# Performance work log

Hardware: AMD Instinct MI355X
Metric: run time of the kernel (lower is better)

## Reference

```python
import jax, jax.numpy as jnp
import numpy as np

B, N, M, K, S, P, H, W = 8, 32, 32, 3, 1, 1, 192, 192
NH = (H + 2 * P - K) // S + 1
NW = (W + 2 * P - K) // S + 1


def setup_inputs() -> dict:
    key = jax.random.key(0)
    ks = jax.random.split(key, 8)
    f = lambda k, sh, sc: jax.random.normal(k, sh, jnp.float32) * sc
    return {
        "x": f(ks[0], (B, N, H, W), 1.0),
        "a1_w": f(ks[1], (K * K, N, K, K), 0.05),  # attention1 conv k x k
        "a1_b": jnp.zeros((K * K,), jnp.float32),
        "a2_w": f(ks[2], (K * K, K * K), 0.1),      # attention1 1x1 conv
        "a2_b": jnp.zeros((K * K,), jnp.float32),
        "a3_w": f(ks[3], (K * K, K * K), 0.1),      # attention1 1x1 conv
        "a3_b": jnp.zeros((K * K,), jnp.float32),
        "b1_w": f(ks[4], (M, N), 0.05),             # attention3 1x1 conv
        "b1_b": jnp.zeros((M,), jnp.float32),
        "b2_w": f(ks[5], (M, M), 0.05),             # attention3 1x1 conv
        "b2_b": jnp.zeros((M,), jnp.float32),
        "weight": f(ks[6], (M, N, K, K), 0.05),     # main conv weight
    }


def _attention1(x, a1_w, a1_b, a2_w, a2_b, a3_w, a3_b):
    # Conv(k) -> ReLU -> Conv1x1 -> ReLU -> Conv1x1 -> Sigmoid; out [B, K*K, NH, NW]
    a = jax.lax.conv_general_dilated(
        x, a1_w, (S, S), [(P, P), (P, P)],
        dimension_numbers=("NCHW", "OIHW", "NCHW"))
    a = jax.nn.relu(a + a1_b[None, :, None, None])
    a = jax.nn.relu(jnp.einsum("oi,bihw->bohw", a2_w, a) + a2_b[None, :, None, None])
    a = jnp.einsum("oi,bihw->bohw", a3_w, a) + a3_b[None, :, None, None]
    return jax.nn.sigmoid(a)


def _unfold(x):
    # torch F.unfold ordering: channel-major, kernel positions inner.
    # returns [B, N, K*K, NH, NW]
    xp = jnp.pad(x, ((0, 0), (0, 0), (P, P), (P, P)))
    cols = [xp[:, :, i:i + (NH - 1) * S + 1:S, j:j + (NW - 1) * S + 1:S]
            for i in range(K) for j in range(K)]
    return jnp.stack(cols, axis=2)


def reference(x, a1_w, a1_b, a2_w, a2_b, a3_w, a3_b, b1_w, b1_b, b2_w, b2_b, weight):
    att = _attention1(x, a1_w, a1_b, a2_w, a2_b, a3_w, a3_b)  # [B, K*K, NH, NW]
    pat = _unfold(x)                                          # [B, N, K*K, NH, NW]
    w = weight.reshape(M, N, K * K)
    # attention-weighted unfold + matmul + fold, fused as one einsum
    y = jnp.einsum("bnphw,bphw,mnp->bmhw", pat, att, w)       # [B, M, NH, NW]
    # attention3 bias: global avg pool -> 1x1 -> ReLU -> 1x1
    pooled = x.mean(axis=(2, 3))                              # [B, N]
    h = jax.nn.relu(pooled @ b1_w.T + b1_b)
    bias = h @ b2_w.T + b2_b                                  # [B, M]
    return y + bias[:, :, None, None]
```

## Files before the change

### kernel.cpp

```cpp
#include <hip/hip_runtime.h>
#include <math.h>

#define B_ 8
#define N_ 32
#define M_ 32
#define HW 192

typedef __attribute__((ext_vector_type(8))) short short8;
typedef __attribute__((ext_vector_type(4))) float float4_;

__device__ inline unsigned short f2bf(float f) {
    unsigned int b = __float_as_uint(f);
    b += 0x7FFF + ((b >> 16) & 1);
    return (unsigned short)(b >> 16);
}
__device__ inline float bf2f(unsigned short u) {
    return __uint_as_float((unsigned int)u << 16);
}

union U8 { short8 s; unsigned int u[4]; };

__global__ __launch_bounds__(256) void pool_prep_kernel(
    const float* __restrict__ x, const float* __restrict__ a1w,
    const float* __restrict__ weight, float* __restrict__ pooled,
    unsigned short* __restrict__ a1A, unsigned short* __restrict__ wA) {
    if (blockIdx.x == 256) {
        int tid = threadIdx.x;
        for (int idx = tid; idx < 9 * 512; idx += 256) {
            int j = idx & 7, l = (idx >> 3) & 63, c = idx >> 9;
            int o = l & 15, n = (l >> 4) * 8 + j;
            float v = (o < 9) ? a1w[(o * N_ + n) * 9 + c] : 0.f;
            a1A[idx] = f2bf(v);
        }
        for (int idx = tid; idx < 9 * 1024; idx += 256) {
            int j = idx & 7, l = (idx >> 3) & 63, mt = (idx >> 9) & 1, c = idx >> 10;
            int m = mt * 16 + (l & 15), n = (l >> 4) * 8 + j;
            wA[idx] = f2bf(weight[(m * N_ + n) * 9 + c]);
        }
        return;
    }
    int bn = blockIdx.x;
    const float4_* p = (const float4_*)(x + (size_t)bn * (HW * HW));
    float s = 0.f;
    for (int i = threadIdx.x; i < (HW * HW) / 4; i += 256) {
        float4_ v = p[i];
        s += (v[0] + v[1]) + (v[2] + v[3]);
    }
#pragma unroll
    for (int off = 32; off > 0; off >>= 1) s += __shfl_down(s, off, 64);
    __shared__ float red[4];
    if ((threadIdx.x & 63) == 0) red[threadIdx.x >> 6] = s;
    __syncthreads();
    if (threadIdx.x == 0)
        pooled[bn] = (red[0] + red[1] + red[2] + red[3]) * (1.f / (HW * HW));
}

__global__ __launch_bounds__(256) void laconv_kernel(
    const float* __restrict__ x, const float* __restrict__ a1b,
    const float* __restrict__ a2w, const float* __restrict__ a2b,
    const float* __restrict__ a3w, const float* __restrict__ a3b,
    const unsigned short* __restrict__ a1A, const unsigned short* __restrict__ wA,
    const float* __restrict__ pooled, const float* __restrict__ b1w,
    const float* __restrict__ b1b, const float* __restrict__ b2w,
    const float* __restrict__ b2b, float* __restrict__ out) {
    __shared__ __align__(16) unsigned short xs[324 * 40];
    __shared__ unsigned short att_s[9 * 264];
    __shared__ float hsh[M_];
    __shared__ __align__(16) float bias_lds[M_];

    const int id = blockIdx.x;
    const int b = id & 7;
    const int t = id >> 3;
    const int bx = t % 12, by = t / 12;
    const int th0 = by * 16, tw0 = bx * 16;
    const int tid = threadIdx.x;
    const int wv = tid >> 6, lane = tid & 63;
    const int tx = lane & 15, ks = lane >> 4;
    const float* xb = x + (size_t)b * N_ * HW * HW;

    float fv[5][8];
    int posv[5], grpv[5];
#pragma unroll
    for (int it0 = 0; it0 < 5; ++it0) {
        int it = tid + it0 * 256;
        int grp = it / 324;
        int pos = it - grp * 324;
        posv[it0] = pos; grpv[it0] = grp;
        int r = pos / 18, cc = pos - r * 18;
        int h = th0 + r - 1, wc = tw0 + cc - 1;
        const float* src = xb + (size_t)(grp * 8) * (HW * HW) + h * HW + wc;
        if (((unsigned)h < HW) && ((unsigned)wc < HW)) {
#pragma unroll
            for (int i = 0; i < 8; ++i) fv[it0][i] = src[i * (HW * HW)];
        } else {
#pragma unroll
            for (int i = 0; i < 8; ++i) fv[it0][i] = 0.f;
        }
    }
    float fr[8];
    int posr = 0;
    if (tid < 16) {
        int it = 1280 + tid;
        int pos = it - 3 * 324;
        posr = pos;
        int r = pos / 18, cc = pos - r * 18;
        int h = th0 + r - 1, wc = tw0 + cc - 1;
        const float* src = xb + (size_t)24 * (HW * HW) + h * HW + wc;
        if (((unsigned)h < HW) && ((unsigned)wc < HW)) {
#pragma unroll
            for (int i = 0; i < 8; ++i) fr[i] = src[i * (HW * HW)];
        } else {
#pragma unroll
            for (int i = 0; i < 8; ++i) fr[i] = 0.f;
        }
    }
#pragma unroll
    for (int it0 = 0; it0 < 5; ++it0) {
        U8 tt;
#pragma unroll
        for (int i = 0; i < 4; ++i)
            tt.u[i] = (unsigned)f2bf(fv[it0][2 * i]) |
                      ((unsigned)f2bf(fv[it0][2 * i + 1]) << 16);
        *(short8*)&xs[posv[it0] * 40 + grpv[it0] * 8] = tt.s;
    }
    if (tid < 16) {
        U8 tt;
#pragma unroll
        for (int i = 0; i < 4; ++i)
            tt.u[i] = (unsigned)f2bf(fr[2 * i]) | ((unsigned)f2bf(fr[2 * i + 1]) << 16);
        *(short8*)&xs[posr * 40 + 24] = tt.s;
    }
    if (tid < M_) {
        float s = b1b[tid];
#pragma unroll
        for (int n = 0; n < N_; n++) s += pooled[b * N_ + n] * b1w[tid * N_ + n];
        hsh[tid] = fmaxf(s, 0.f);
    }
    __syncthreads();
    if (tid < M_) {
        float s2 = b2b[tid];
#pragma unroll
        for (int q = 0; q < M_; q++) s2 += hsh[q] * b2w[tid * M_ + q];
        bias_lds[tid] = s2;
    }

    const int pb = (wv * 4) * 720 + tx * 40 + ks * 8;
    const float4_ zero4 = {0.f, 0.f, 0.f, 0.f};

    float4_ aacc[4];
#pragma unroll
    for (int g = 0; g < 4; ++g) aacc[g] = zero4;
#pragma unroll
    for (int c = 0; c < 9; ++c) {
        short8 aA = ((const short8*)a1A)[c * 64 + lane];
        const int coff = (c / 3) * 720 + (c % 3) * 40;
#pragma unroll
        for (int g = 0; g < 4; ++g) {
            short8 bP = *(const short8*)&xs[pb + g * 720 + coff];
            aacc[g] = __builtin_amdgcn_mfma_f32_16x16x32_bf16(aA, bP, aacc[g], 0, 0, 0);
        }
    }
#pragma unroll
    for (int g = 0; g < 4; ++g) {
#pragma unroll
        for (int reg = 0; reg < 4; ++reg) {
            int o = ks * 4 + reg;
            if (o < 9) att_s[o * 264 + (wv * 4 + g) * 16 + tx] = f2bf(aacc[g][reg]);
        }
    }
    __syncthreads();

    float t1[9], t2[9], attv[9];
#pragma unroll
    for (int o = 0; o < 9; ++o)
        t1[o] = fmaxf(bf2f(att_s[o * 264 + tid]) + a1b[o], 0.f);
#pragma unroll
    for (int o2 = 0; o2 < 9; ++o2) {
        float s = a2b[o2];
#pragma unroll
        for (int o = 0; o < 9; ++o) s += a2w[o2 * 9 + o] * t1[o];
        t2[o2] = fmaxf(s, 0.f);
    }
#pragma unroll
    for (int o3 = 0; o3 < 9; ++o3) {
        float s = a3b[o3];
#pragma unroll
        for (int o2 = 0; o2 < 9; ++o2) s += a3w[o3 * 9 + o2] * t2[o2];
        attv[o3] = 1.f / (1.f + __expf(-s));
    }
#pragma unroll
    for (int p = 0; p < 9; ++p) att_s[p * 264 + tid] = f2bf(attv[p]);
    __syncthreads();

    float4_ acc0[4], acc1[4];
#pragma unroll
    for (int g = 0; g < 4; ++g) { acc0[g] = zero4; acc1[g] = zero4; }
#pragma unroll
    for (int c = 0; c < 9; ++c) {
        short8 w0 = ((const short8*)wA)[c * 128 + lane];
        short8 w1 = ((const short8*)wA)[c * 128 + 64 + lane];
        const int coff = (c / 3) * 720 + (c % 3) * 40;
#pragma unroll
        for (int g = 0; g < 4; ++g) {
            short8 bP = *(const short8*)&xs[pb + g * 720 + coff];
            float av = bf2f(att_s[c * 264 + (wv * 4 + g) * 16 + tx]);
            float4_ av4 = {av, av, av, av};
            float4_ z0 = __builtin_amdgcn_mfma_f32_16x16x32_bf16(w0, bP, zero4, 0, 0, 0);
            float4_ z1 = __builtin_amdgcn_mfma_f32_16x16x32_bf16(w1, bP, zero4, 0, 0, 0);
            acc0[g] = acc0[g] + av4 * z0;
            acc1[g] = acc1[g] + av4 * z1;
        }
    }

    const int wc = tw0 + tx;
    float4_ bv0 = *(const float4_*)&bias_lds[ks * 4];
    float4_ bv1 = *(const float4_*)&bias_lds[16 + ks * 4];
#pragma unroll
    for (int g = 0; g < 4; ++g) {
        int h = th0 + wv * 4 + g;
#pragma unroll
        for (int reg = 0; reg < 4; ++reg) {
            int m0 = ks * 4 + reg;
            out[((b * M_ + m0) * HW + h) * HW + wc] = acc0[g][reg] + bv0[reg];
            out[((b * M_ + m0 + 16) * HW + h) * HW + wc] = acc1[g][reg] + bv1[reg];
        }
    }
}

extern "C" void kernel_launch(void* const* d_in, const int* in_sizes, int n_in,
                              void* d_out, int out_size, void* d_ws,
                              size_t ws_size, hipStream_t stream) {
    const float* x   = (const float*)d_in[0];
    const float* a1w = (const float*)d_in[1];
    const float* a1b = (const float*)d_in[2];
    const float* a2w = (const float*)d_in[3];
    const float* a2b = (const float*)d_in[4];
    const float* a3w = (const float*)d_in[5];
    const float* a3b = (const float*)d_in[6];
    const float* b1w = (const float*)d_in[7];
    const float* b1b = (const float*)d_in[8];
    const float* b2w = (const float*)d_in[9];
    const float* b2b = (const float*)d_in[10];
    const float* wgt = (const float*)d_in[11];
    float* out = (float*)d_out;

    char* ws = (char*)d_ws;
    float* pooled        = (float*)(ws);
    unsigned short* a1A  = (unsigned short*)(ws + 2048);
    unsigned short* wAf  = (unsigned short*)(ws + 11264);

    pool_prep_kernel<<<dim3(B_ * N_ + 1), dim3(256), 0, stream>>>(
        x, a1w, wgt, pooled, a1A, wAf);
    laconv_kernel<<<dim3(12 * 12 * B_), dim3(256), 0, stream>>>(
        x, a1b, a2w, a2b, a3w, a3b, a1A, wAf, pooled, b1w, b1b, b2w, b2b, out);
    (void)in_sizes; (void)n_in; (void)out_size; (void)ws_size;
}
```

Measured before the change: 139.3 us.

## Pre-transpose input to channel-last bf16 in pool kernel, load tiles vectorized

The pooling kernel now also writes a channel-last bf16 copy of x (32 channels per pixel, 64 bytes each) and emits per-row-chunk partial sums instead of full means. The main conv kernel then loads each halo pixel with four 16-byte loads in place of 32 strided fp32 loads, and uses a channel-group-major LDS layout with smaller padding. Pooled sums are reduced inside the conv kernel, and part of the bias MLP is moved later to overlap with other work. The cost is an extra full read and write of a bf16 copy of x through global memory, plus a launch-bounds occupancy hint.

```diff
diff --git a/kernel.cpp b/kernel.cpp
--- a/kernel.cpp
+++ b/kernel.cpp
@@ -20,52 +20,75 @@
 
 union U8 { short8 s; unsigned int u[4]; };
 
-__global__ __launch_bounds__(256) void pool_prep_kernel(
+__global__ __launch_bounds__(192) void pool_prep_kernel(
     const float* __restrict__ x, const float* __restrict__ a1w,
-    const float* __restrict__ weight, float* __restrict__ pooled,
-    unsigned short* __restrict__ a1A, unsigned short* __restrict__ wA) {
-    if (blockIdx.x == 256) {
-        int tid = threadIdx.x;
-        for (int idx = tid; idx < 9 * 512; idx += 256) {
+    const float* __restrict__ weight, float* __restrict__ partial,
+    unsigned short* __restrict__ a1A, unsigned short* __restrict__ wA,
+    unsigned short* __restrict__ xt) {
+    const int id = blockIdx.x;
+    const int tid = threadIdx.x;
+    if (id == 256) {
+        for (int idx = tid; idx < 9 * 512; idx += 192) {
             int j = idx & 7, l = (idx >> 3) & 63, c = idx >> 9;
             int o = l & 15, n = (l >> 4) * 8 + j;
             float v = (o < 9) ? a1w[(o * N_ + n) * 9 + c] : 0.f;
             a1A[idx] = f2bf(v);
         }
-        for (int idx = tid; idx < 9 * 1024; idx += 256) {
+        for (int idx = tid; idx < 9 * 1024; idx += 192) {
             int j = idx & 7, l = (idx >> 3) & 63, mt = (idx >> 9) & 1, c = idx >> 10;
             int m = mt * 16 + (l & 15), n = (l >> 4) * 8 + j;
             wA[idx] = f2bf(weight[(m * N_ + n) * 9 + c]);
         }
         return;
     }
-    int bn = blockIdx.x;
-    const float4_* p = (const float4_*)(x + (size_t)bn * (HW * HW));
-    float s = 0.f;
-    for (int i = threadIdx.x; i < (HW * HW) / 4; i += 256) {
-        float4_ v = p[i];
-        s += (v[0] + v[1]) + (v[2] + v[3]);
-    }
-#pragma unroll
-    for (int off = 32; off > 0; off >>= 1) s += __shfl_down(s, off, 64);
-    __shared__ float red[4];
-    if ((threadIdx.x & 63) == 0) red[threadIdx.x >> 6] = s;
-    __syncthreads();
-    if (threadIdx.x == 0)
-        pooled[bn] = (red[0] + red[1] + red[2] + red[3]) * (1.f / (HW * HW));
-}
-
-__global__ __launch_bounds__(256) void laconv_kernel(
-    const float* __restrict__ x, const float* __restrict__ a1b,
+    const int b = id >> 5, hc = id & 31;
+    const float* xb = x + (size_t)b * N_ * (HW * HW);
+    float sum[32];
+#pragma unroll
+    for (int n = 0; n < 32; ++n) sum[n] = 0.f;
+    for (int h6 = 0; h6 < 6; ++h6) {
+        const int h = hc * 6 + h6;
+        float v[32];
+#pragma unroll
+        for (int n = 0; n < 32; ++n) {
+            v[n] = xb[n * (HW * HW) + h * HW + tid];
+            sum[n] += v[n];
+        }
+        U8 tq[4];
+#pragma unroll
+        for (int q = 0; q < 4; ++q)
+#pragma unroll
+            for (int i = 0; i < 4; ++i)
+                tq[q].u[i] = (unsigned)f2bf(v[q * 8 + 2 * i]) |
+                             ((unsigned)f2bf(v[q * 8 + 2 * i + 1]) << 16);
+        short8* dst = (short8*)&xt[(((size_t)b * HW + h) * HW + tid) * 32];
+        dst[0] = tq[0].s; dst[1] = tq[1].s; dst[2] = tq[2].s; dst[3] = tq[3].s;
+    }
+    __shared__ float red[3][32];
+    const int wv = tid >> 6, lane = tid & 63;
+#pragma unroll
+    for (int n = 0; n < 32; ++n) {
+        float s = sum[n];
+#pragma unroll
+        for (int off = 32; off > 0; off >>= 1) s += __shfl_down(s, off, 64);
+        if (lane == 0) red[wv][n] = s;
+    }
+    __syncthreads();
+    if (tid < 32)
+        partial[(b * 32 + hc) * 32 + tid] = red[0][tid] + red[1][tid] + red[2][tid];
+}
+
+__global__ __launch_bounds__(256, 6) void laconv_kernel(
+    const unsigned short* __restrict__ xt, const float* __restrict__ a1b,
     const float* __restrict__ a2w, const float* __restrict__ a2b,
     const float* __restrict__ a3w, const float* __restrict__ a3b,
     const unsigned short* __restrict__ a1A, const unsigned short* __restrict__ wA,
-    const float* __restrict__ pooled, const float* __restrict__ b1w,
+    const float* __restrict__ partial, const float* __restrict__ b1w,
     const float* __restrict__ b1b, const float* __restrict__ b2w,
     const float* __restrict__ b2b, float* __restrict__ out) {
-    __shared__ __align__(16) unsigned short xs[324 * 40];
+    __shared__ __align__(16) unsigned short xs[4 * 324 * 8];
     __shared__ unsigned short att_s[9 * 264];
-    __shared__ float hsh[M_];
+    __shared__ float pooled_s[N_], hsh[M_];
     __shared__ __align__(16) float bias_lds[M_];
 
     const int id = blockIdx.x;
@@ -76,75 +99,54 @@
     const int tid = threadIdx.x;
     const int wv = tid >> 6, lane = tid & 63;
     const int tx = lane & 15, ks = lane >> 4;
-    const float* xb = x + (size_t)b * N_ * HW * HW;
-
-    float fv[5][8];
-    int posv[5], grpv[5];
-#pragma unroll
-    for (int it0 = 0; it0 < 5; ++it0) {
-        int it = tid + it0 * 256;
-        int grp = it / 324;
-        int pos = it - grp * 324;
-        posv[it0] = pos; grpv[it0] = grp;
-        int r = pos / 18, cc = pos - r * 18;
-        int h = th0 + r - 1, wc = tw0 + cc - 1;
-        const float* src = xb + (size_t)(grp * 8) * (HW * HW) + h * HW + wc;
-        if (((unsigned)h < HW) && ((unsigned)wc < HW)) {
-#pragma unroll
-            for (int i = 0; i < 8; ++i) fv[it0][i] = src[i * (HW * HW)];
+
+    const unsigned short* xtb = xt + (size_t)b * (HW * HW) * 32;
+    short8 ra[4], rb[4];
+    {
+        int pos = tid, r = pos / 18, cc = pos - r * 18;
+        int h = th0 + r - 1, w = tw0 + cc - 1;
+        if (((unsigned)h < HW) && ((unsigned)w < HW)) {
+            const short8* src = (const short8*)&xtb[(size_t)(h * HW + w) * 32];
+            ra[0] = src[0]; ra[1] = src[1]; ra[2] = src[2]; ra[3] = src[3];
         } else {
 #pragma unroll
-            for (int i = 0; i < 8; ++i) fv[it0][i] = 0.f;
-        }
-    }
-    float fr[8];
-    int posr = 0;
-    if (tid < 16) {
-        int it = 1280 + tid;
-        int pos = it - 3 * 324;
-        posr = pos;
-        int r = pos / 18, cc = pos - r * 18;
-        int h = th0 + r - 1, wc = tw0 + cc - 1;
-        const float* src = xb + (size_t)24 * (HW * HW) + h * HW + wc;
-        if (((unsigned)h < HW) && ((unsigned)wc < HW)) {
-#pragma unroll
-            for (int i = 0; i < 8; ++i) fr[i] = src[i * (HW * HW)];
+            for (int g = 0; g < 4; ++g) ra[g] = (short8)(short)0;
+        }
+    }
+    const bool hasB = tid < 324 - 256;
+    if (hasB) {
+        int pos = 256 + tid, r = pos / 18, cc = pos - r * 18;
+        int h = th0 + r - 1, w = tw0 + cc - 1;
+        if (((unsigned)h < HW) && ((unsigned)w < HW)) {
+            const short8* src = (const short8*)&xtb[(size_t)(h * HW + w) * 32];
+            rb[0] = src[0]; rb[1] = src[1]; rb[2] = src[2]; rb[3] = src[3];
         } else {
 #pragma unroll
-            for (int i = 0; i < 8; ++i) fr[i] = 0.f;
-        }
-    }
-#pragma unroll
-    for (int it0 = 0; it0 < 5; ++it0) {
-        U8 tt;
-#pragma unroll
-        for (int i = 0; i < 4; ++i)
-            tt.u[i] = (unsigned)f2bf(fv[it0][2 * i]) |
-                      ((unsigned)f2bf(fv[it0][2 * i + 1]) << 16);
-        *(short8*)&xs[posv[it0] * 40 + grpv[it0] * 8] = tt.s;
-    }
-    if (tid < 16) {
-        U8 tt;
-#pragma unroll
-        for (int i = 0; i < 4; ++i)
-            tt.u[i] = (unsigned)f2bf(fr[2 * i]) | ((unsigned)f2bf(fr[2 * i + 1]) << 16);
-        *(short8*)&xs[posr * 40 + 24] = tt.s;
-    }
+            for (int g = 0; g < 4; ++g) rb[g] = (short8)(short)0;
+        }
+    }
+    float ps = 0.f;
+    if (tid < N_) {
+#pragma unroll
+        for (int c = 0; c < 32; ++c) ps += partial[(b * 32 + c) * 32 + tid];
+    }
+#pragma unroll
+    for (int g = 0; g < 4; ++g) *(short8*)&xs[g * 2592 + tid * 8] = ra[g];
+    if (hasB) {
+#pragma unroll
+        for (int g = 0; g < 4; ++g) *(short8*)&xs[g * 2592 + (256 + tid) * 8] = rb[g];
+    }
+    if (tid < N_) pooled_s[tid] = ps * (1.f / (HW * HW));
+    __syncthreads();
+
     if (tid < M_) {
         float s = b1b[tid];
 #pragma unroll
-        for (int n = 0; n < N_; n++) s += pooled[b * N_ + n] * b1w[tid * N_ + n];
+        for (int n = 0; n < N_; n++) s += pooled_s[n] * b1w[tid * N_ + n];
         hsh[tid] = fmaxf(s, 0.f);
     }
-    __syncthreads();
-    if (tid < M_) {
-        float s2 = b2b[tid];
-#pragma unroll
-        for (int q = 0; q < M_; q++) s2 += hsh[q] * b2w[tid * M_ + q];
-        bias_lds[tid] = s2;
-    }
-
-    const int pb = (wv * 4) * 720 + tx * 40 + ks * 8;
+
+    const int pb = ks * 2592 + wv * 576 + tx * 8;
     const float4_ zero4 = {0.f, 0.f, 0.f, 0.f};
 
     float4_ aacc[4];
@@ -153,10 +155,10 @@
 #pragma unroll
     for (int c = 0; c < 9; ++c) {
         short8 aA = ((const short8*)a1A)[c * 64 + lane];
-        const int coff = (c / 3) * 720 + (c % 3) * 40;
+        const int coff = (c / 3) * 144 + (c % 3) * 8;
 #pragma unroll
         for (int g = 0; g < 4; ++g) {
-            short8 bP = *(const short8*)&xs[pb + g * 720 + coff];
+            short8 bP = *(const short8*)&xs[pb + g * 144 + coff];
             aacc[g] = __builtin_amdgcn_mfma_f32_16x16x32_bf16(aA, bP, aacc[g], 0, 0, 0);
         }
     }
@@ -170,6 +172,13 @@
     }
     __syncthreads();
 
+    if (tid < M_) {
+        float s2 = b2b[tid];
+#pragma unroll
+        for (int q = 0; q < M_; q++) s2 += hsh[q] * b2w[tid * M_ + q];
+        bias_lds[tid] = s2;
+    }
+
     float t1[9], t2[9], attv[9];
 #pragma unroll
     for (int o = 0; o < 9; ++o)
@@ -199,10 +208,10 @@
     for (int c = 0; c < 9; ++c) {
         short8 w0 = ((const short8*)wA)[c * 128 + lane];
         short8 w1 = ((const short8*)wA)[c * 128 + 64 + lane];
-        const int coff = (c / 3) * 720 + (c % 3) * 40;
+        const int coff = (c / 3) * 144 + (c % 3) * 8;
 #pragma unroll
         for (int g = 0; g < 4; ++g) {
-            short8 bP = *(const short8*)&xs[pb + g * 720 + coff];
+            short8 bP = *(const short8*)&xs[pb + g * 144 + coff];
             float av = bf2f(att_s[c * 264 + (wv * 4 + g) * 16 + tx]);
             float4_ av4 = {av, av, av, av};
             float4_ z0 = __builtin_amdgcn_mfma_f32_16x16x32_bf16(w0, bP, zero4, 0, 0, 0);
@@ -245,13 +254,14 @@
     float* out = (float*)d_out;
 
     char* ws = (char*)d_ws;
-    float* pooled        = (float*)(ws);
-    unsigned short* a1A  = (unsigned short*)(ws + 2048);
-    unsigned short* wAf  = (unsigned short*)(ws + 11264);
-
-    pool_prep_kernel<<<dim3(B_ * N_ + 1), dim3(256), 0, stream>>>(
-        x, a1w, wgt, pooled, a1A, wAf);
+    float* partial       = (float*)(ws);
+    unsigned short* a1A  = (unsigned short*)(ws + 32768);
+    unsigned short* wAf  = (unsigned short*)(ws + 41984);
+    unsigned short* xt   = (unsigned short*)(ws + 65536);
+
+    pool_prep_kernel<<<dim3(257), dim3(192), 0, stream>>>(
+        x, a1w, wgt, partial, a1A, wAf, xt);
     laconv_kernel<<<dim3(12 * 12 * B_), dim3(256), 0, stream>>>(
-        x, a1b, a2w, a2b, a3w, a3b, a1A, wAf, pooled, b1w, b1b, b2w, b2b, out);
+        xt, a1b, a2w, a2b, a3w, a3b, a1A, wAf, partial, b1w, b1b, b2w, b2b, out);
     (void)in_sizes; (void)n_in; (void)out_size; (void)ws_size;
 }
```

Result: slower. 151.7 us (+8.9%).
